# Kernel tuning notes

Measured on AMD Instinct MI355X. Metric: run time of the kernel, lower is better.

## Reference

```python
import jax, jax.numpy as jnp
import numpy as np

TEMPERATURE = 0.1
BASE_TEMPERATURE = 0.07
EPS = 1e-10


def setup_inputs() -> dict:
    key = jax.random.key(0)
    k1, k2 = jax.random.split(key)
    # feats_: [total_classes=64, n_view=128, feat_dim=256] sampled anchor features
    feats_ = jax.random.normal(k1, (64, 128, 256), dtype=jnp.float32)
    # labels_: class id per anchor group (21-class dataset -> repeats across groups)
    labels_ = jax.random.randint(k2, (64,), 0, 21, dtype=jnp.int32)
    return {"feats_": feats_, "labels_": labels_}


def reference(feats_, labels_):
    anchor_num, n_view, d = feats_.shape
    N = anchor_num * n_view
    # torch.cat(torch.unbind(feats_, dim=1), dim=0): view-major flattening
    cf = jnp.transpose(feats_, (1, 0, 2)).reshape(N, d)  # [N, d]
    # labels for the flattened ordering (mask.repeat tiles the [A,A] eq-mask)
    big_labels = jnp.tile(labels_, n_view)  # [N]

    logits = jnp.matmul(cf, cf.T) / TEMPERATURE  # [N, N]
    logits = logits - jax.lax.stop_gradient(jnp.max(logits, axis=1, keepdims=True))

    mask = (big_labels[:, None] == big_labels[None, :]).astype(jnp.float32)
    neg_mask = 1.0 - mask                       # negatives BEFORE removing diagonal
    mask = mask * (1.0 - jnp.eye(N, dtype=jnp.float32))  # positives exclude self

    exp_logits = jnp.exp(logits)
    neg_logits = jnp.sum(exp_logits * neg_mask, axis=1, keepdims=True)  # [N, 1]
    log_prob = logits - jnp.log(exp_logits + neg_logits + EPS)
    mean_log_prob_pos = jnp.sum(mask * log_prob, axis=1) / jnp.sum(mask, axis=1)
    loss = jnp.mean(-(TEMPERATURE / BASE_TEMPERATURE) * mean_log_prob_pos)
    return loss
```

## Files before the change

kernel.cpp:

```cpp
#include <hip/hip_runtime.h>
#include <hip/hip_bf16.h>

#define N_ROWS 8192
#define DIM 256
#define NANCH 64
#define NVIEW 128
#define APS 16
#define NPART 8

typedef __attribute__((ext_vector_type(8))) short bf16x8;
typedef __attribute__((ext_vector_type(4))) float f32x4;
typedef __attribute__((ext_vector_type(16))) float f32x16;
typedef __attribute__((ext_vector_type(4))) float float4v;
typedef __attribute__((ext_vector_type(4))) unsigned short ushort4v;

__device__ __forceinline__ unsigned short f2bf(float x) {
  union { float f; unsigned int u; } c; c.f = x;
  unsigned int u = c.u;
  unsigned int r = (u + 0x7fffu + ((u >> 16) & 1u)) >> 16;
  return (unsigned short)r;
}

__device__ __forceinline__ float bf2f(unsigned short b) {
  union { unsigned int u; float f; } c; c.u = ((unsigned int)b) << 16;
  return c.f;
}

__device__ __forceinline__ void gload_lds16(const void* g, void* l) {
  __builtin_amdgcn_global_load_lds(
      (const __attribute__((address_space(1))) unsigned int*)g,
      (__attribute__((address_space(3))) unsigned int*)l, 16, 0, 0);
}

__global__ void cast_diag_kernel(const float4v* __restrict__ in,
                                 ushort4v* __restrict__ out,
                                 float* __restrict__ diag) {
  const int w = threadIdx.x >> 6;
  const int l = threadIdx.x & 63;
  const int row = blockIdx.x * 4 + w;
  const float s = 3.16227766016838f;
  float4v v = in[row * 64 + l];
  ushort4v o;
  o.x = f2bf(v.x * s);
  o.y = f2bf(v.y * s);
  o.z = f2bf(v.z * s);
  o.w = f2bf(v.w * s);
  out[row * 64 + l] = o;
  float c0 = bf2f(o.x), c1 = bf2f(o.y), c2 = bf2f(o.z), c3 = bf2f(o.w);
  float ss = c0 * c0 + c1 * c1 + c2 * c2 + c3 * c3;
#pragma unroll
  for (int st = 1; st < 64; st <<= 1) ss += __shfl_xor(ss, st);
  if (l == 0) diag[row] = ss;
}

__global__ __launch_bounds__(256, 2) void pcl_negsum(
    const unsigned short* __restrict__ Xb, const int* __restrict__ labels,
    const float* __restrict__ diag, float* __restrict__ ns_partial) {
  const int rb = blockIdx.x & 63;
  const int part = blockIdx.x >> 6;
  const int strip = part >> 1;
  const int half = part & 1;
  const int tid = threadIdx.x;
  const int wid = tid >> 6;
  const int lane = tid & 63;
  const int l31 = lane & 31;
  const int khalf = lane >> 5;
  const int rg = wid >> 1;
  const int cg = wid & 1;

  __shared__ __align__(16) unsigned short buf[2][64 * DIM];
  __shared__ float sdiag[128];
  __shared__ float nsacc[128];
  __shared__ int slab[NANCH];

  if (tid < NANCH) slab[tid] = labels[tid];
  if (tid < 128) nsacc[tid] = 0.f;
  if (tid >= 128) sdiag[tid - 128] = diag[rb * 128 + tid - 128];
  __syncthreads();
  const int myLab = slab[rb];

  bf16x8 afrag[2][16];
#pragma unroll
  for (int ri = 0; ri < 2; ++ri) {
#pragma unroll
    for (int ks = 0; ks < 16; ++ks) {
      const unsigned short* p =
          Xb + (size_t)(rb * 128 + rg * 64 + ri * 32 + l31) * DIM + ks * 16 + khalf * 8;
      afrag[ri][ks] = *(const bf16x8*)p;
      asm volatile("" : "+v"(afrag[ri][ks]));
    }
  }

  float thr;
  {
    float d = sdiag[rg * 64 + lane];
#pragma unroll
    for (int st = 1; st < 64; st <<= 1) d = fminf(d, __shfl_xor(d, st));
    thr = d - 40.f;
  }

  const int srcbase = lane * DIM + wid * 8;
  const unsigned short* asrc0 =
      Xb + ((size_t)(strip * APS) * NVIEW + half * 64) * DIM;

#pragma unroll
  for (int i = 0; i < 8; ++i)
    gload_lds16(asrc0 + srcbase + i * 32, (char*)&buf[0][0] + wid * 1024 + i * 4096);
  __syncthreads();

  const int boff = khalf * 1024 + cg * 512 + l31 * 16;

  int cb = 0;
  for (int a = 0; a < APS; ++a) {
    if (a + 1 < APS) {
      const unsigned short* src = asrc0 + (size_t)(a + 1) * NVIEW * DIM;
#pragma unroll
      for (int i = 0; i < 8; ++i)
        gload_lds16(src + srcbase + i * 32, (char*)&buf[cb ^ 1][0] + wid * 1024 + i * 4096);
    }

    const char* bufc = (const char*)&buf[cb][0];
    f32x16 a0A = {}, a0B = {}, a1A = {}, a1B = {};
#pragma unroll
    for (int ks = 0; ks < 16; ++ks) {
      bf16x8 bfr = *(const bf16x8*)(bufc + ks * 2048 + boff);
      if (ks < 8) {
        a0A = __builtin_amdgcn_mfma_f32_32x32x16_bf16(afrag[0][ks], bfr, a0A, 0, 0, 0);
        a1A = __builtin_amdgcn_mfma_f32_32x32x16_bf16(afrag[1][ks], bfr, a1A, 0, 0, 0);
      } else {
        a0B = __builtin_amdgcn_mfma_f32_32x32x16_bf16(afrag[0][ks], bfr, a0B, 0, 0, 0);
        a1B = __builtin_amdgcn_mfma_f32_32x32x16_bf16(afrag[1][ks], bfr, a1B, 0, 0, 0);
      }
    }

    if (slab[strip * APS + a] != myLab) {
      f32x16 c0 = a0A + a0B;
      f32x16 c1 = a1A + a1B;
      float vmax = c0[0];
#pragma unroll
      for (int r = 1; r < 16; ++r) vmax = fmaxf(vmax, c0[r]);
#pragma unroll
      for (int r = 0; r < 16; ++r) vmax = fmaxf(vmax, c1[r]);
      if (__builtin_expect(__any(vmax > thr), 0)) {
#pragma unroll
        for (int t2 = 0; t2 < 2; ++t2) {
#pragma unroll
          for (int r = 0; r < 16; ++r) {
            const int rloc = (r & 3) + 8 * (r >> 2) + 4 * khalf;
            const int row = rg * 64 + t2 * 32 + rloc;
            float v = t2 ? c1[r] : c0[r];
            float mr = sdiag[row];
            float e = (v > mr - 40.f) ? __expf(v - mr) : 0.f;
#pragma unroll
            for (int st = 1; st < 32; st <<= 1) e += __shfl_xor(e, st);
            if (l31 == 0) atomicAdd(&nsacc[row], e);
          }
        }
      }
    }
    __syncthreads();
    cb ^= 1;
  }

  if (tid < 128)
    ns_partial[part * N_ROWS + rb * 128 + tid] = nsacc[tid];
}

__global__ __launch_bounds__(512, 4) void pcl_pos(
    const unsigned short* __restrict__ Xb, const int* __restrict__ labels,
    const float* __restrict__ diag, const float* __restrict__ ns_partial,
    float* __restrict__ partials) {
  const int blk = blockIdx.x;
  const int r0 = blk * 32;
  const int tid = threadIdx.x;
  const int wid = tid >> 6;
  const int lane = tid & 63;
  const int lo = lane & 15;
  const int hi = lane >> 4;
  const int cq = wid & 3;
  const int bq = wid >> 2;

  __shared__ int slab[NANCH];
  __shared__ float sred[8][32];
  __shared__ float smf[32];
  __shared__ float snsf[32];
  __shared__ float slog[32];
  __shared__ int poslist[NANCH];
  __shared__ int scnt;

  if (tid < NANCH) slab[tid] = labels[tid];
  if (tid >= 64 && tid < 96) {
    int r = tid - 64;
    smf[r] = diag[r0 + r];
    float s = 0.f;
#pragma unroll
    for (int p = 0; p < NPART; ++p) s += ns_partial[p * N_ROWS + r0 + r];
    snsf[r] = s;
    slog[r] = __logf(s + 1e-10f);
  }
  if (tid == 0) {
    int La0 = labels[blk >> 2];
    int c = 0;
    for (int b = 0; b < NANCH; ++b)
      if (labels[b] == La0) poslist[c++] = b;
    scnt = c;
  }
  __syncthreads();

  bf16x8 afrag[2][8];
#pragma unroll
  for (int ri = 0; ri < 2; ++ri) {
#pragma unroll
    for (int ks = 0; ks < 8; ++ks) {
      const unsigned short* p = Xb + (r0 + ri * 16 + lo) * DIM + ks * 32 + hi * 8;
      afrag[ri][ks] = *(const bf16x8*)p;
      asm volatile("" : "+v"(afrag[ri][ks]));
    }
  }

  const int cnt = scnt;
  float pos[8];
#pragma unroll
  for (int t = 0; t < 8; ++t) pos[t] = 0.f;

  for (int p = bq; p < cnt; p += 2) {
    const int b = poslist[p];
    const int c0 = b * NVIEW + cq * 32;
    f32x4 acc[2][2];
#pragma unroll
    for (int ri = 0; ri < 2; ++ri)
#pragma unroll
      for (int ci = 0; ci < 2; ++ci)
        acc[ri][ci] = (f32x4){0.f, 0.f, 0.f, 0.f};

#pragma unroll
    for (int ks = 0; ks < 8; ++ks) {
      bf16x8 b0 = *(const bf16x8*)(Xb + (c0 + lo) * DIM + ks * 32 + hi * 8);
      bf16x8 b1 = *(const bf16x8*)(Xb + (c0 + 16 + lo) * DIM + ks * 32 + hi * 8);
      acc[0][0] = __builtin_amdgcn_mfma_f32_16x16x32_bf16(afrag[0][ks], b0, acc[0][0], 0, 0, 0);
      acc[0][1] = __builtin_amdgcn_mfma_f32_16x16x32_bf16(afrag[0][ks], b1, acc[0][1], 0, 0, 0);
      acc[1][0] = __builtin_amdgcn_mfma_f32_16x16x32_bf16(afrag[1][ks], b0, acc[1][0], 0, 0, 0);
      acc[1][1] = __builtin_amdgcn_mfma_f32_16x16x32_bf16(afrag[1][ks], b1, acc[1][1], 0, 0, 0);
    }

#pragma unroll
    for (int ri = 0; ri < 2; ++ri) {
#pragma unroll
      for (int ci = 0; ci < 2; ++ci) {
#pragma unroll
        for (int reg = 0; reg < 4; ++reg) {
          const int t = ri * 4 + reg;
          const int row = ri * 16 + hi * 4 + reg;
          int grow = r0 + row;
          int gcol = c0 + ci * 16 + lo;
          if (grow != gcol) {
            float d = acc[ri][ci][reg] - smf[row];
            float lp;
            if (__builtin_expect(d > -45.f, 0))
              lp = d - __logf(__expf(d) + snsf[row] + 1e-10f);
            else
              lp = d - slog[row];
            pos[t] += lp;
          }
        }
      }
    }
  }

#pragma unroll
  for (int t = 0; t < 8; ++t) {
#pragma unroll
    for (int st = 1; st < 16; st <<= 1) pos[t] += __shfl_xor(pos[t], st);
  }
  if (lo == 0) {
#pragma unroll
    for (int ri = 0; ri < 2; ++ri)
#pragma unroll
      for (int reg = 0; reg < 4; ++reg)
        sred[wid][ri * 16 + hi * 4 + reg] = pos[ri * 4 + reg];
  }
  __syncthreads();

  const float poscnt = (float)(cnt * NVIEW - 1);
  if (tid < 32) {
    float P = 0.f;
#pragma unroll
    for (int w = 0; w < 8; ++w) P += sred[w][tid];
    smf[tid] = P / poscnt;
  }
  __syncthreads();
  if (tid == 0) {
    float s = 0.f;
    for (int r = 0; r < 32; ++r) s += smf[r];
    partials[blk] = s;
  }
}

__global__ void final_reduce(const float* __restrict__ partials, float* __restrict__ out) {
  __shared__ float s[256];
  int t = threadIdx.x;
  s[t] = partials[t];
  __syncthreads();
  for (int st = 128; st > 0; st >>= 1) {
    if (t < st) s[t] += s[t + st];
    __syncthreads();
  }
  if (t == 0) out[0] = -(0.1f / 0.07f) * s[0] / (float)N_ROWS;
}

extern "C" void kernel_launch(void* const* d_in, const int* in_sizes, int n_in,
                              void* d_out, int out_size, void* d_ws, size_t ws_size,
                              hipStream_t stream) {
  const float* feats = (const float*)d_in[0];
  const int* labels = (const int*)d_in[1];
  float* out = (float*)d_out;

  char* base = (char*)d_ws;
  unsigned short* Xb = (unsigned short*)d_ws;
  float* diag = (float*)(base + (size_t)N_ROWS * DIM * 2);
  float* ns_partial = (float*)(base + (size_t)N_ROWS * DIM * 2 + N_ROWS * 4);
  float* partials = (float*)(base + (size_t)N_ROWS * DIM * 2 + N_ROWS * 4 +
                             NPART * N_ROWS * 4);

  cast_diag_kernel<<<N_ROWS / 4, 256, 0, stream>>>((const float4v*)feats,
                                                   (ushort4v*)Xb, diag);
  pcl_negsum<<<NANCH * NPART, 256, 0, stream>>>(Xb, labels, diag, ns_partial);
  pcl_pos<<<N_ROWS / 32, 512, 0, stream>>>(Xb, labels, diag, ns_partial, partials);
  final_reduce<<<1, 256, 0, stream>>>(partials, out);
}
```

Baseline: 78.29 us.

## Restructure negsum kernel into 512-thread blocks with 4-stage LDS ring pipeline

The negative-sum kernel now uses 512-thread blocks covering 256 anchor rows each, so every staged column tile is reused across twice as many rows. Column tiles stream through a 4-slot LDS ring that keeps three tiles in flight, using explicit vmcnt waits and raw s_barrier in place of a double buffer with full __syncthreads. The inner MFMA loop is interleaved across the two K halves and runs at raised wave priority. This aims to hide global-to-LDS latency and halve redundant B-tile loads, at the cost of 128KB of LDS per block, which limits occupancy.

Result: faster. 75.35 us (-3.8%).

```diff
diff --git a/kernel.cpp b/kernel.cpp
--- a/kernel.cpp
+++ b/kernel.cpp
@@ -5,7 +5,6 @@
 #define DIM 256
 #define NANCH 64
 #define NVIEW 128
-#define APS 16
 #define NPART 8
 
 typedef __attribute__((ext_vector_type(8))) short bf16x8;
@@ -53,13 +52,13 @@
   if (l == 0) diag[row] = ss;
 }
 
-__global__ __launch_bounds__(256, 2) void pcl_negsum(
+__global__ __launch_bounds__(512, 2) void pcl_negsum(
     const unsigned short* __restrict__ Xb, const int* __restrict__ labels,
     const float* __restrict__ diag, float* __restrict__ ns_partial) {
-  const int rb = blockIdx.x & 63;
-  const int part = blockIdx.x >> 6;
-  const int strip = part >> 1;
-  const int half = part & 1;
+  const int bx = blockIdx.x;
+  const int rbp = bx & 31;
+  const int part = bx >> 5;
+  const int abase = part * 8;
   const int tid = threadIdx.x;
   const int wid = tid >> 6;
   const int lane = tid & 63;
@@ -67,17 +66,17 @@
   const int khalf = lane >> 5;
   const int rg = wid >> 1;
   const int cg = wid & 1;
-
-  __shared__ __align__(16) unsigned short buf[2][64 * DIM];
-  __shared__ float sdiag[128];
-  __shared__ float nsacc[128];
+  const int R0 = rbp * 256;
+
+  __shared__ __align__(16) unsigned short ring[4 * 64 * DIM];
+  __shared__ float sdiag[256];
+  __shared__ float nsacc[256];
   __shared__ int slab[NANCH];
 
   if (tid < NANCH) slab[tid] = labels[tid];
-  if (tid < 128) nsacc[tid] = 0.f;
-  if (tid >= 128) sdiag[tid - 128] = diag[rb * 128 + tid - 128];
-  __syncthreads();
-  const int myLab = slab[rb];
+  if (tid < 256) { sdiag[tid] = diag[R0 + tid]; nsacc[tid] = 0.f; }
+  __syncthreads();
+  const int myLab = slab[rbp * 2 + (rg >> 1)];
 
   bf16x8 afrag[2][16];
 #pragma unroll
@@ -85,11 +84,14 @@
 #pragma unroll
     for (int ks = 0; ks < 16; ++ks) {
       const unsigned short* p =
-          Xb + (size_t)(rb * 128 + rg * 64 + ri * 32 + l31) * DIM + ks * 16 + khalf * 8;
+          Xb + (size_t)(R0 + rg * 64 + ri * 32 + l31) * DIM + ks * 16 + khalf * 8;
       afrag[ri][ks] = *(const bf16x8*)p;
-      asm volatile("" : "+v"(afrag[ri][ks]));
     }
   }
+#pragma unroll
+  for (int ri = 0; ri < 2; ++ri)
+#pragma unroll
+    for (int ks = 0; ks < 16; ++ks) asm volatile("" : "+v"(afrag[ri][ks]));
 
   float thr;
   {
@@ -99,71 +101,78 @@
     thr = d - 40.f;
   }
 
-  const int srcbase = lane * DIM + wid * 8;
-  const unsigned short* asrc0 =
-      Xb + ((size_t)(strip * APS) * NVIEW + half * 64) * DIM;
-
-#pragma unroll
-  for (int i = 0; i < 8; ++i)
-    gload_lds16(asrc0 + srcbase + i * 32, (char*)&buf[0][0] + wid * 1024 + i * 4096);
-  __syncthreads();
-
-  const int boff = khalf * 1024 + cg * 512 + l31 * 16;
-
-  int cb = 0;
-  for (int a = 0; a < APS; ++a) {
-    if (a + 1 < APS) {
-      const unsigned short* src = asrc0 + (size_t)(a + 1) * NVIEW * DIM;
-#pragma unroll
-      for (int i = 0; i < 8; ++i)
-        gload_lds16(src + srcbase + i * 32, (char*)&buf[cb ^ 1][0] + wid * 1024 + i * 4096);
-    }
-
-    const char* bufc = (const char*)&buf[cb][0];
-    f32x16 a0A = {}, a0B = {}, a1A = {}, a1B = {};
-#pragma unroll
-    for (int ks = 0; ks < 16; ++ks) {
-      bf16x8 bfr = *(const bf16x8*)(bufc + ks * 2048 + boff);
-      if (ks < 8) {
-        a0A = __builtin_amdgcn_mfma_f32_32x32x16_bf16(afrag[0][ks], bfr, a0A, 0, 0, 0);
-        a1A = __builtin_amdgcn_mfma_f32_32x32x16_bf16(afrag[1][ks], bfr, a1A, 0, 0, 0);
-      } else {
-        a0B = __builtin_amdgcn_mfma_f32_32x32x16_bf16(afrag[0][ks], bfr, a0B, 0, 0, 0);
-        a1B = __builtin_amdgcn_mfma_f32_32x32x16_bf16(afrag[1][ks], bfr, a1B, 0, 0, 0);
-      }
-    }
-
-    if (slab[strip * APS + a] != myLab) {
-      f32x16 c0 = a0A + a0B;
-      f32x16 c1 = a1A + a1B;
-      float vmax = c0[0];
-#pragma unroll
-      for (int r = 1; r < 16; ++r) vmax = fmaxf(vmax, c0[r]);
-#pragma unroll
-      for (int r = 0; r < 16; ++r) vmax = fmaxf(vmax, c1[r]);
-      if (__builtin_expect(__any(vmax > thr), 0)) {
-#pragma unroll
-        for (int t2 = 0; t2 < 2; ++t2) {
-#pragma unroll
-          for (int r = 0; r < 16; ++r) {
-            const int rloc = (r & 3) + 8 * (r >> 2) + 4 * khalf;
-            const int row = rg * 64 + t2 * 32 + rloc;
-            float v = t2 ? c1[r] : c0[r];
-            float mr = sdiag[row];
-            float e = (v > mr - 40.f) ? __expf(v - mr) : 0.f;
-#pragma unroll
-            for (int st = 1; st < 32; st <<= 1) e += __shfl_xor(e, st);
-            if (l31 == 0) atomicAdd(&nsacc[row], e);
-          }
-        }
-      }
-    }
-    __syncthreads();
-    cb ^= 1;
-  }
-
-  if (tid < 128)
-    ns_partial[part * N_ROWS + rb * 128 + tid] = nsacc[tid];
+  char* const L0 = (char*)&ring[0];
+
+#define STAGE(H)                                                                \
+  do {                                                                          \
+    const unsigned short* _s =                                                  \
+        Xb + (size_t)((abase + ((H) >> 1)) * NVIEW + ((H) & 1) * 64 + lane) *   \
+                 DIM + wid * 8;                                                 \
+    char* _d = L0 + ((H) & 3) * 32768 + wid * 1024;                             \
+    gload_lds16(_s, _d);                                                        \
+    gload_lds16(_s + 64, _d + 8192);                                            \
+    gload_lds16(_s + 128, _d + 16384);                                          \
+    gload_lds16(_s + 192, _d + 24576);                                          \
+  } while (0)
+
+  STAGE(0);
+  STAGE(1);
+  STAGE(2);
+
+#define ITER(S, VN)                                                             \
+  do {                                                                          \
+    if ((S) + 3 < 16) STAGE((S) + 3);                                           \
+    asm volatile("s_waitcnt vmcnt(" #VN ")");                                   \
+    __builtin_amdgcn_sched_barrier(0);                                          \
+    __builtin_amdgcn_s_barrier();                                               \
+    __builtin_amdgcn_sched_barrier(0);                                          \
+    const char* _sb =                                                           \
+        L0 + ((S) & 3) * 32768 + khalf * 1024 + cg * 512 + l31 * 16;            \
+    f32x16 a0A = {}, a0B = {}, a1A = {}, a1B = {};                              \
+    __builtin_amdgcn_s_setprio(1);                                              \
+    _Pragma("unroll") for (int ks = 0; ks < 8; ++ks) {                          \
+      bf16x8 b0 = *(const bf16x8*)(_sb + ks * 2048);                            \
+      bf16x8 b1 = *(const bf16x8*)(_sb + (ks + 8) * 2048);                      \
+      a0A = __builtin_amdgcn_mfma_f32_32x32x16_bf16(afrag[0][ks], b0, a0A, 0, 0, 0); \
+      a1A = __builtin_amdgcn_mfma_f32_32x32x16_bf16(afrag[1][ks], b0, a1A, 0, 0, 0); \
+      a0B = __builtin_amdgcn_mfma_f32_32x32x16_bf16(afrag[0][ks + 8], b1, a0B, 0, 0, 0); \
+      a1B = __builtin_amdgcn_mfma_f32_32x32x16_bf16(afrag[1][ks + 8], b1, a1B, 0, 0, 0); \
+    }                                                                           \
+    __builtin_amdgcn_s_setprio(0);                                              \
+    if (slab[abase + ((S) >> 1)] != myLab) {                                    \
+      f32x16 c0 = a0A + a0B;                                                    \
+      f32x16 c1 = a1A + a1B;                                                    \
+      float vmax = fmaxf(c0[0], c1[0]);                                         \
+      _Pragma("unroll") for (int r = 1; r < 16; ++r)                            \
+          vmax = fmaxf(vmax, fmaxf(c0[r], c1[r]));                              \
+      if (__builtin_expect(__any(vmax > thr), 0)) {                             \
+        _Pragma("unroll") for (int t2 = 0; t2 < 2; ++t2) {                      \
+          _Pragma("unroll") for (int r = 0; r < 16; ++r) {                      \
+            const int rloc = (r & 3) + 8 * (r >> 2) + 4 * khalf;                \
+            const int row = rg * 64 + t2 * 32 + rloc;                           \
+            float v = t2 ? c1[r] : c0[r];                                       \
+            float mr = sdiag[row];                                              \
+            float e = (v > mr - 40.f) ? __expf(v - mr) : 0.f;                   \
+            _Pragma("unroll") for (int st = 1; st < 32; st <<= 1)               \
+                e += __shfl_xor(e, st);                                         \
+            if (l31 == 0) atomicAdd(&nsacc[row], e);                            \
+          }                                                                     \
+        }                                                                       \
+      }                                                                         \
+    }                                                                           \
+    __builtin_amdgcn_s_barrier();                                               \
+  } while (0)
+
+  ITER(0, 12);  ITER(1, 12);  ITER(2, 12);  ITER(3, 12);
+  ITER(4, 12);  ITER(5, 12);  ITER(6, 12);  ITER(7, 12);
+  ITER(8, 12);  ITER(9, 12);  ITER(10, 12); ITER(11, 12);
+  ITER(12, 12); ITER(13, 8);  ITER(14, 4);  ITER(15, 0);
+
+#undef ITER
+#undef STAGE
+
+  __syncthreads();
+  if (tid < 256) ns_partial[part * N_ROWS + R0 + tid] = nsacc[tid];
 }
 
 __global__ __launch_bounds__(512, 4) void pcl_pos(
@@ -324,7 +333,7 @@
 
   cast_diag_kernel<<<N_ROWS / 4, 256, 0, stream>>>((const float4v*)feats,
                                                    (ushort4v*)Xb, diag);
-  pcl_negsum<<<NANCH * NPART, 256, 0, stream>>>(Xb, labels, diag, ns_partial);
+  pcl_negsum<<<32 * NPART, 512, 0, stream>>>(Xb, labels, diag, ns_partial);
   pcl_pos<<<N_ROWS / 32, 512, 0, stream>>>(Xb, labels, diag, ns_partial, partials);
   final_reduce<<<1, 256, 0, stream>>>(partials, out);
 }
```
